# Performance work log

Measured on AMD Instinct MI355X. Metric: run time of the kernel, lower is better.

## Reference

```python
import jax, jax.numpy as jnp
import numpy as np

TAU = 0.1
EPS_NORM = 1e-12  # torch F.normalize clamp
EPS_DEN = 1e-6


def setup_inputs() -> dict:
    key = jax.random.key(0)
    k1, k2, k3, k4 = jax.random.split(key, 4)
    B, C, H, W = 4, 128, 64, 64
    feat_A = jax.random.normal(k1, (B, C, H, W), dtype=jnp.float32)
    feat_B = jax.random.normal(k2, (B, C, H, W), dtype=jnp.float32)
    H_mat = jax.random.normal(k3, (B, 3, 3), dtype=jnp.float32)
    valid_mask = jax.random.uniform(k4, (B, H, W), dtype=jnp.float32)
    return {"feat_A": feat_A, "feat_B": feat_B, "H_mat": H_mat, "valid_mask": valid_mask}


def _l2_normalize(x, axis):
    n = jnp.sqrt(jnp.sum(x * x, axis=axis, keepdims=True))
    return x / jnp.maximum(n, EPS_NORM)


def reference(feat_A, feat_B, H_mat, valid_mask):
    B, C, H, W = feat_A.shape
    HW = H * W
    fA = _l2_normalize(feat_A.reshape(B, C, HW), axis=1)  # [B, C, HW]
    fB = _l2_normalize(feat_B.reshape(B, C, HW), axis=1)  # [B, C, HW]
    # sim[b, n, m] = <fA[:, :, n], fB[:, :, m]> / tau
    sim = jnp.einsum('bcn,bcm->bnm', fA, fB) / TAU  # [B, HW, HW]
    # torch CE with input [B, HW, HW], labels arange(HW): class axis is 1,
    # so logits for position k are the column sim[b, :, k], target = k.
    lse = jax.nn.logsumexp(sim, axis=1)               # [B, HW] (over class axis)
    diag = jnp.einsum('bkk->bk', sim)                 # sim[b, k, k]
    loss = lse - diag                                  # [B, HW], per-position CE
    mask_flat = valid_mask.reshape(B, HW)
    return (loss * mask_flat).sum() / (mask_flat.sum() + EPS_DEN)
```

## Files before the change

### kernel.cpp

```cpp
#include <hip/hip_runtime.h>
#include <math.h>

#define BB 4
#define CC 128
#define HW 4096
#define SCF 3.798282565f

typedef short short8 __attribute__((ext_vector_type(8)));
typedef float f32x4 __attribute__((ext_vector_type(4)));

static __device__ inline unsigned short f2bf(float f) {
  unsigned int u = __float_as_uint(f);
  u += 0x7fffu + ((u >> 16) & 1u);
  return (unsigned short)(u >> 16);
}

__global__ __launch_bounds__(256) void k_prep(const float* __restrict__ fA,
                                              const float* __restrict__ fB,
                                              unsigned short* __restrict__ fAn,
                                              unsigned short* __restrict__ fBn,
                                              float* __restrict__ diag,
                                              float* __restrict__ expsum,
                                              float* __restrict__ acc) {
  __shared__ float sA[32 * 129];
  __shared__ float sB[32 * 129];
  __shared__ float red[3 * 256];

  const int bid = blockIdx.x;
  const int b   = bid >> 7;
  const int n0  = (bid & 127) * 32;
  const int tid = threadIdx.x;
  const int cR  = tid >> 5;
  const int n   = tid & 31;

  if (bid == 0 && tid == 0) { acc[0] = 0.f; acc[1] = 0.f; ((unsigned*)acc)[2] = 0u; }

  const float* pa = fA + (size_t)b * CC * HW + n0 + n;
  const float* pb = fB + (size_t)b * CC * HW + n0 + n;

  float ssa = 0.f, ssb = 0.f, dot = 0.f;
  #pragma unroll
  for (int it = 0; it < 16; ++it) {
    int c = it * 8 + cR;
    float va = pa[(size_t)c * HW];
    float vb = pb[(size_t)c * HW];
    sA[n * 129 + c] = va;
    sB[n * 129 + c] = vb;
    ssa = fmaf(va, va, ssa);
    ssb = fmaf(vb, vb, ssb);
    dot = fmaf(va, vb, dot);
  }
  red[tid] = ssa; red[256 + tid] = ssb; red[512 + tid] = dot;
  __syncthreads();

  if (tid < 32) {
    float sa = 0.f, sb = 0.f, dt = 0.f;
    #pragma unroll
    for (int k = 0; k < 8; ++k) {
      sa += red[k * 32 + tid];
      sb += red[256 + k * 32 + tid];
      dt += red[512 + k * 32 + tid];
    }
    float ia = 1.f / fmaxf(sqrtf(sa), 1e-12f);
    float ib = 1.f / fmaxf(sqrtf(sb), 1e-12f);
    int gidx = b * HW + n0 + tid;
    diag[gidx]   = dt * ia * ib * 10.f;
    expsum[gidx] = 0.f;
    red[tid]      = ia * SCF;
    red[32 + tid] = ib * SCF;
  }
  __syncthreads();

  #pragma unroll
  for (int r = 0; r < 2; ++r) {
    int L  = r * 256 + tid;
    int nn = L >> 4;
    int q  = L & 15;
    int c0 = (q ^ (nn & 7)) * 8;
    size_t base = ((size_t)b * HW + n0 + nn) * 128 + q * 8;
    {
      float sc = red[nn];
      const float* s = &sA[nn * 129 + c0];
      uint4 v;
      v.x = f2bf(s[0]*sc) | ((unsigned)f2bf(s[1]*sc) << 16);
      v.y = f2bf(s[2]*sc) | ((unsigned)f2bf(s[3]*sc) << 16);
      v.z = f2bf(s[4]*sc) | ((unsigned)f2bf(s[5]*sc) << 16);
      v.w = f2bf(s[6]*sc) | ((unsigned)f2bf(s[7]*sc) << 16);
      *(uint4*)(fAn + base) = v;
    }
    {
      float sc = red[32 + nn];
      const float* s = &sB[nn * 129 + c0];
      uint4 v;
      v.x = f2bf(s[0]*sc) | ((unsigned)f2bf(s[1]*sc) << 16);
      v.y = f2bf(s[2]*sc) | ((unsigned)f2bf(s[3]*sc) << 16);
      v.z = f2bf(s[4]*sc) | ((unsigned)f2bf(s[5]*sc) << 16);
      v.w = f2bf(s[6]*sc) | ((unsigned)f2bf(s[7]*sc) << 16);
      *(uint4*)(fBn + base) = v;
    }
  }
}

__global__ __launch_bounds__(256, 2) void k_main(const unsigned short* __restrict__ fAn,
                                                 const unsigned short* __restrict__ fBn,
                                                 float* __restrict__ expsum,
                                                 const float* __restrict__ diag,
                                                 const float* __restrict__ mask,
                                                 float* __restrict__ acc,
                                                 float* __restrict__ out) {
  __shared__ unsigned short sB[16384];
  __shared__ unsigned short sA[2][8192];

  const int bid = blockIdx.x;
  const int x   = bid & 7;
  const int t   = bid >> 3;
  const int b   = x & 3;
  const int nq  = (x >> 2) | ((t & 1) << 1);
  const int mt  = t >> 1;
  const int m0  = mt * 128;
  const int nbase = nq * 1024;
  const int tid = threadIdx.x;

  const int wv   = tid >> 6;
  const int lane = tid & 63;
  const int ml   = lane & 15;
  const int g    = lane >> 4;
  const int wn   = (wv & 1) * 32;
  const int wm   = (wv >> 1) * 64;

  const unsigned short* gAbase = fAn + ((size_t)b * HW + nbase) * 128;

  {
    const unsigned short* gB = fBn + ((size_t)b * HW + m0) * 128;
    #pragma unroll
    for (int r = 0; r < 8; ++r) {
      int L = r * 256 + tid;
      __builtin_amdgcn_global_load_lds(
          (const __attribute__((address_space(1))) unsigned int*)(gB + (size_t)L * 8),
          (__attribute__((address_space(3))) unsigned int*)(sB + L * 8), 16, 0, 0);
    }
    #pragma unroll
    for (int r = 0; r < 4; ++r) {
      int L = r * 256 + tid;
      __builtin_amdgcn_global_load_lds(
          (const __attribute__((address_space(1))) unsigned int*)(gAbase + (size_t)L * 8),
          (__attribute__((address_space(3))) unsigned int*)(sA[0] + L * 8), 16, 0, 0);
    }
  }
  __syncthreads();

  short8 bf[4][4];
  #pragma unroll
  for (int kc = 0; kc < 4; ++kc) {
    int q = kc * 4 + g;
    #pragma unroll
    for (int j = 0; j < 4; ++j) {
      int nb = wm + j * 16 + ml;
      bf[kc][j] = *(const short8*)(sB + nb * 128 + ((q ^ (nb & 7)) * 8));
    }
  }

  float colAcc[4] = {0.f, 0.f, 0.f, 0.f};

  for (int it = 0; it < 16; ++it) {
    if (it < 15) {
      const unsigned short* gA = gAbase + (size_t)(it + 1) * 8192;
      unsigned short* dst = sA[(it + 1) & 1];
      #pragma unroll
      for (int r = 0; r < 4; ++r) {
        int L = r * 256 + tid;
        __builtin_amdgcn_global_load_lds(
            (const __attribute__((address_space(1))) unsigned int*)(gA + (size_t)L * 8),
            (__attribute__((address_space(3))) unsigned int*)(dst + L * 8), 16, 0, 0);
      }
    }

    const unsigned short* bufc = sA[it & 1];
    f32x4 acc4[2][4] = {};
    #pragma unroll
    for (int kc = 0; kc < 4; ++kc) {
      int q = kc * 4 + g;
      short8 af0, af1;
      {
        int na = wn + ml;
        af0 = *(const short8*)(bufc + na * 128 + ((q ^ (na & 7)) * 8));
        na = wn + 16 + ml;
        af1 = *(const short8*)(bufc + na * 128 + ((q ^ (na & 7)) * 8));
      }
      #pragma unroll
      for (int j = 0; j < 4; ++j) {
        acc4[0][j] = __builtin_amdgcn_mfma_f32_16x16x32_bf16(af0, bf[kc][j], acc4[0][j], 0, 0, 0);
        acc4[1][j] = __builtin_amdgcn_mfma_f32_16x16x32_bf16(af1, bf[kc][j], acc4[1][j], 0, 0, 0);
      }
    }
    #pragma unroll
    for (int j = 0; j < 4; ++j) {
      float e = 0.f;
      #pragma unroll
      for (int i = 0; i < 2; ++i)
        #pragma unroll
        for (int r = 0; r < 4; ++r)
          e += exp2f(acc4[i][j][r]);
      colAcc[j] += e;
    }

    __syncthreads();
  }

  #pragma unroll
  for (int j = 0; j < 4; ++j) {
    float e = colAcc[j];
    e += __shfl_xor(e, 16, 64);
    e += __shfl_xor(e, 32, 64);
    if (lane < 16)
      atomicAdd(&expsum[(size_t)b * HW + m0 + wm + j * 16 + lane], e);
  }

  unsigned* flag = (unsigned*)sA;
  __syncthreads();
  if (tid == 0) {
    __threadfence();
    flag[0] = (atomicAdd((unsigned*)(acc + 2), 1u) == 511u) ? 1u : 0u;
  }
  __syncthreads();
  if (flag[0]) {
    float num = 0.f, den = 0.f;
    #pragma unroll 4
    for (int i = tid; i < BB * HW; i += 256) {
      float es = __hip_atomic_load(expsum + i, __ATOMIC_RELAXED, __HIP_MEMORY_SCOPE_AGENT);
      float mv = mask[i];
      num = fmaf(mv, __logf(es) - diag[i], num);
      den += mv;
    }
    #pragma unroll
    for (int off = 32; off; off >>= 1) {
      num += __shfl_down(num, off, 64);
      den += __shfl_down(den, off, 64);
    }
    float* red = (float*)sB;
    if (lane == 0) { red[wv] = num; red[8 + wv] = den; }
    __syncthreads();
    if (tid == 0) {
      float n = red[0] + red[1] + red[2] + red[3];
      float d = red[8] + red[9] + red[10] + red[11];
      out[0] = n / (d + 1e-6f);
    }
  }
}

extern "C" void kernel_launch(void* const* d_in, const int* in_sizes, int n_in,
                              void* d_out, int out_size, void* d_ws, size_t ws_size,
                              hipStream_t stream) {
  const float* feat_A = (const float*)d_in[0];
  const float* feat_B = (const float*)d_in[1];
  const float* vmask  = (const float*)d_in[3];

  unsigned short* fAn = (unsigned short*)d_ws;
  unsigned short* fBn = fAn + (size_t)BB * HW * CC;
  float* diag   = (float*)(fBn + (size_t)BB * HW * CC);
  float* expsum = diag + BB * HW;
  float* acc    = expsum + BB * HW;
  float* out    = (float*)d_out;

  k_prep<<<512, 256, 0, stream>>>(feat_A, feat_B, fAn, fBn, diag, expsum, acc);
  k_main<<<512, 256, 0, stream>>>(fAn, fBn, expsum, diag, vmask, acc, out);
}
```

Before: 115.8 us.

## Load A fragments directly from global into registers, drop LDS A buffer

k_main no longer stages A tiles through double-buffered LDS with block-wide barriers. Each wave reads its own A rows straight from global memory into registers, prefetching one chunk ahead in a ping-pong scheme. The grid doubles to 1024 blocks with 512 n-rows each, and occupancy is raised to 3 blocks per CU because LDS use shrinks. The aim is to remove the per-iteration __syncthreads and the LDS traffic, at the cost of more uncoalesced global/L2 reads and twice as many atomic adds to expsum.

```diff
diff --git a/kernel.cpp b/kernel.cpp
--- a/kernel.cpp
+++ b/kernel.cpp
@@ -101,7 +101,7 @@
   }
 }
 
-__global__ __launch_bounds__(256, 2) void k_main(const unsigned short* __restrict__ fAn,
+__global__ __launch_bounds__(256, 3) void k_main(const unsigned short* __restrict__ fAn,
                                                  const unsigned short* __restrict__ fBn,
                                                  float* __restrict__ expsum,
                                                  const float* __restrict__ diag,
@@ -109,26 +109,25 @@
                                                  float* __restrict__ acc,
                                                  float* __restrict__ out) {
   __shared__ unsigned short sB[16384];
-  __shared__ unsigned short sA[2][8192];
+  __shared__ float redS[16];
+  __shared__ unsigned flagS;
 
   const int bid = blockIdx.x;
   const int x   = bid & 7;
   const int t   = bid >> 3;
   const int b   = x & 3;
-  const int nq  = (x >> 2) | ((t & 1) << 1);
-  const int mt  = t >> 1;
+  const int nq  = ((x >> 2) << 2) | (t & 3);
+  const int mt  = t >> 2;
   const int m0  = mt * 128;
-  const int nbase = nq * 1024;
+  const int n0  = nq * 512;
   const int tid = threadIdx.x;
 
   const int wv   = tid >> 6;
   const int lane = tid & 63;
   const int ml   = lane & 15;
   const int g    = lane >> 4;
-  const int wn   = (wv & 1) * 32;
-  const int wm   = (wv >> 1) * 64;
-
-  const unsigned short* gAbase = fAn + ((size_t)b * HW + nbase) * 128;
+  const int wm   = (wv & 1) * 64;
+  const int wn   = (wv >> 1) * 256;
 
   {
     const unsigned short* gB = fBn + ((size_t)b * HW + m0) * 128;
@@ -139,72 +138,67 @@
           (const __attribute__((address_space(1))) unsigned int*)(gB + (size_t)L * 8),
           (__attribute__((address_space(3))) unsigned int*)(sB + L * 8), 16, 0, 0);
     }
-    #pragma unroll
-    for (int r = 0; r < 4; ++r) {
-      int L = r * 256 + tid;
-      __builtin_amdgcn_global_load_lds(
-          (const __attribute__((address_space(1))) unsigned int*)(gAbase + (size_t)L * 8),
-          (__attribute__((address_space(3))) unsigned int*)(sA[0] + L * 8), 16, 0, 0);
-    }
   }
   __syncthreads();
 
   short8 bf[4][4];
   #pragma unroll
   for (int kc = 0; kc < 4; ++kc) {
-    int q = kc * 4 + g;
     #pragma unroll
     for (int j = 0; j < 4; ++j) {
       int nb = wm + j * 16 + ml;
-      bf[kc][j] = *(const short8*)(sB + nb * 128 + ((q ^ (nb & 7)) * 8));
-    }
-  }
+      bf[kc][j] = *(const short8*)(sB + nb * 128 + (((kc * 4 + g) ^ (nb & 7)) * 8));
+    }
+  }
+
+  const unsigned short* pA = fAn + ((size_t)b * HW + n0 + wn + ml) * 128;
+  int xoff[4];
+  #pragma unroll
+  for (int kc = 0; kc < 4; ++kc) xoff[kc] = ((kc * 4 + g) ^ (ml & 7)) * 8;
 
   float colAcc[4] = {0.f, 0.f, 0.f, 0.f};
-
-  for (int it = 0; it < 16; ++it) {
-    if (it < 15) {
-      const unsigned short* gA = gAbase + (size_t)(it + 1) * 8192;
-      unsigned short* dst = sA[(it + 1) & 1];
-      #pragma unroll
-      for (int r = 0; r < 4; ++r) {
-        int L = r * 256 + tid;
-        __builtin_amdgcn_global_load_lds(
-            (const __attribute__((address_space(1))) unsigned int*)(gA + (size_t)L * 8),
-            (__attribute__((address_space(3))) unsigned int*)(dst + L * 8), 16, 0, 0);
-      }
-    }
-
-    const unsigned short* bufc = sA[it & 1];
-    f32x4 acc4[2][4] = {};
-    #pragma unroll
-    for (int kc = 0; kc < 4; ++kc) {
-      int q = kc * 4 + g;
-      short8 af0, af1;
-      {
-        int na = wn + ml;
-        af0 = *(const short8*)(bufc + na * 128 + ((q ^ (na & 7)) * 8));
-        na = wn + 16 + ml;
-        af1 = *(const short8*)(bufc + na * 128 + ((q ^ (na & 7)) * 8));
-      }
-      #pragma unroll
-      for (int j = 0; j < 4; ++j) {
-        acc4[0][j] = __builtin_amdgcn_mfma_f32_16x16x32_bf16(af0, bf[kc][j], acc4[0][j], 0, 0, 0);
-        acc4[1][j] = __builtin_amdgcn_mfma_f32_16x16x32_bf16(af1, bf[kc][j], acc4[1][j], 0, 0, 0);
-      }
-    }
-    #pragma unroll
-    for (int j = 0; j < 4; ++j) {
-      float e = 0.f;
-      #pragma unroll
-      for (int i = 0; i < 2; ++i)
+  short8 afA[4], afB[4];
+
+  #pragma unroll
+  for (int kc = 0; kc < 4; ++kc)
+    afA[kc] = *(const short8*)(pA + xoff[kc]);
+
+  #pragma unroll
+  for (int c = 0; c < 16; c += 2) {
+    #pragma unroll
+    for (int kc = 0; kc < 4; ++kc)
+      afB[kc] = *(const short8*)(pA + (size_t)(c + 1) * 2048 + xoff[kc]);
+    {
+      f32x4 a4[4] = {};
+      #pragma unroll
+      for (int kc = 0; kc < 4; ++kc)
+        #pragma unroll
+        for (int j = 0; j < 4; ++j)
+          a4[j] = __builtin_amdgcn_mfma_f32_16x16x32_bf16(afA[kc], bf[kc][j], a4[j], 0, 0, 0);
+      #pragma unroll
+      for (int j = 0; j < 4; ++j)
         #pragma unroll
         for (int r = 0; r < 4; ++r)
-          e += exp2f(acc4[i][j][r]);
-      colAcc[j] += e;
-    }
-
-    __syncthreads();
+          colAcc[j] += exp2f(a4[j][r]);
+    }
+    if (c + 2 < 16) {
+      #pragma unroll
+      for (int kc = 0; kc < 4; ++kc)
+        afA[kc] = *(const short8*)(pA + (size_t)(c + 2) * 2048 + xoff[kc]);
+    }
+    {
+      f32x4 a4[4] = {};
+      #pragma unroll
+      for (int kc = 0; kc < 4; ++kc)
+        #pragma unroll
+        for (int j = 0; j < 4; ++j)
+          a4[j] = __builtin_amdgcn_mfma_f32_16x16x32_bf16(afB[kc], bf[kc][j], a4[j], 0, 0, 0);
+      #pragma unroll
+      for (int j = 0; j < 4; ++j)
+        #pragma unroll
+        for (int r = 0; r < 4; ++r)
+          colAcc[j] += exp2f(a4[j][r]);
+    }
   }
 
   #pragma unroll
@@ -216,14 +210,13 @@
       atomicAdd(&expsum[(size_t)b * HW + m0 + wm + j * 16 + lane], e);
   }
 
-  unsigned* flag = (unsigned*)sA;
   __syncthreads();
   if (tid == 0) {
     __threadfence();
-    flag[0] = (atomicAdd((unsigned*)(acc + 2), 1u) == 511u) ? 1u : 0u;
-  }
-  __syncthreads();
-  if (flag[0]) {
+    flagS = (atomicAdd((unsigned*)(acc + 2), 1u) == 1023u) ? 1u : 0u;
+  }
+  __syncthreads();
+  if (flagS) {
     float num = 0.f, den = 0.f;
     #pragma unroll 4
     for (int i = tid; i < BB * HW; i += 256) {
@@ -237,12 +230,11 @@
       num += __shfl_down(num, off, 64);
       den += __shfl_down(den, off, 64);
     }
-    float* red = (float*)sB;
-    if (lane == 0) { red[wv] = num; red[8 + wv] = den; }
+    if (lane == 0) { redS[wv] = num; redS[8 + wv] = den; }
     __syncthreads();
     if (tid == 0) {
-      float n = red[0] + red[1] + red[2] + red[3];
-      float d = red[8] + red[9] + red[10] + red[11];
+      float n = redS[0] + redS[1] + redS[2] + redS[3];
+      float d = redS[8] + redS[9] + redS[10] + redS[11];
       out[0] = n / (d + 1e-6f);
     }
   }
@@ -262,6 +254,6 @@
   float* acc    = expsum + BB * HW;
   float* out    = (float*)d_out;
 
-  k_prep<<<512, 256, 0, stream>>>(feat_A, feat_B, fAn, fBn, diag, expsum, acc);
-  k_main<<<512, 256, 0, stream>>>(fAn, fBn, expsum, diag, vmask, acc, out);
-}
+  k_prep<<<512,  256, 0, stream>>>(feat_A, feat_B, fAn, fBn, diag, expsum, acc);
+  k_main<<<1024, 256, 0, stream>>>(fAn, fBn, expsum, diag, vmask, acc, out);
+}
```

Measured after the change: 163.3 us. 41.0% more time.
